# Optimization experiments

Measured on AMD Instinct MI355X. Metric: run time of the kernel, lower is better.

## Reference

```python
import jax, jax.numpy as jnp
import numpy as np

N_TOKENS = 8192
D_MODEL = 1024
D_HIDDEN = 4096
N_EXPERTS = 8
TOP_K = 2


def setup_inputs() -> dict:
    key = jax.random.key(0)
    ks = jax.random.split(key, 7)
    s = 0.02
    return {
        "x": jax.random.normal(ks[0], (N_TOKENS, D_MODEL), dtype=jnp.float32),
        "gate_w": jax.random.normal(ks[1], (D_MODEL, N_EXPERTS), dtype=jnp.float32) * s,
        "gate_b": jnp.zeros((N_EXPERTS,), dtype=jnp.float32),
        "w1": jax.random.normal(ks[2], (N_EXPERTS, D_MODEL, D_HIDDEN), dtype=jnp.float32) * s,
        "b1": jnp.zeros((N_EXPERTS, D_HIDDEN), dtype=jnp.float32),
        "w2": jax.random.normal(ks[3], (N_EXPERTS, D_HIDDEN, D_MODEL), dtype=jnp.float32) * s,
        "b2": jnp.zeros((N_EXPERTS, D_MODEL), dtype=jnp.float32),
    }


def reference(x, gate_w, gate_b, w1, b1, w2, b2):
    # Gating: softmax over experts, then top-k routing
    gate_scores = jax.nn.softmax(x @ gate_w + gate_b, axis=-1)        # [N, E]
    topk_vals, topk_idx = jax.lax.top_k(gate_scores, TOP_K)          # [N, K]

    # Combine weights: sum of topk_vals scattered to expert slots
    onehot = jax.nn.one_hot(topk_idx, N_EXPERTS, dtype=x.dtype)      # [N, K, E]
    combine = jnp.einsum('nk,nke->ne', topk_vals, onehot)            # [N, E]

    # Dense expert evaluation (math identical to masked dispatch: unselected
    # experts receive weight 0 in `combine`).
    h = jax.nn.relu(jnp.einsum('nd,edh->neh', x, w1) + b1)           # [N, E, H]
    expert_out = jnp.einsum('neh,ehd->ned', h, w2) + b2              # [N, E, D]
    output = jnp.einsum('ned,ne->nd', expert_out, combine)           # [N, D]

    # Load-balancing loss from routing counts
    load = jnp.sum(onehot, axis=(0, 1))                              # [E]
    load_balancing_loss = jnp.sum((load / jnp.sum(load)) ** 2)
    return output, load_balancing_loss
```

## Files before the change

### kernel.cpp

```cpp
#include <hip/hip_runtime.h>

#define D_MODEL   1024
#define D_HIDDEN  4096
#define N_EXPERTS 8
#define N_TOKENS  8192
#define NASSIGN   (N_TOKENS * 2)
#define PADCAP    (NASSIGN + N_EXPERTS * 128)
#define ROWT      (PADCAP / 128)

typedef unsigned short u16;
typedef __bf16 bf16x8 __attribute__((ext_vector_type(8)));
typedef float  f32x4  __attribute__((ext_vector_type(4)));

__device__ __forceinline__ u16 f2bf(float f) {
  union { float f; unsigned u; } c; c.f = f;
  unsigned u = c.u;
  u = (u + 0x7fffu + ((u >> 16) & 1u)) >> 16;
  return (u16)u;
}

__device__ __forceinline__ void async16(const void* g, void* l) {
  __builtin_amdgcn_global_load_lds(
      (const __attribute__((address_space(1))) unsigned int*)g,
      (__attribute__((address_space(3))) unsigned int*)l, 16, 0, 0);
}

__global__ __launch_bounds__(64) void gating_kernel(
    const float* __restrict__ x, const float* __restrict__ gw,
    const float* __restrict__ gb, int* __restrict__ counts,
    int* __restrict__ tok_idx, float* __restrict__ tok_w)
{
  const int n = blockIdx.x;
  const int lane = threadIdx.x;
  float acc[8] = {0.f,0.f,0.f,0.f,0.f,0.f,0.f,0.f};
  for (int d = lane; d < D_MODEL; d += 64) {
    float xv = x[(size_t)n * D_MODEL + d];
    const float4* g = (const float4*)&gw[d * 8];
    float4 g0 = g[0], g1 = g[1];
    acc[0] += xv * g0.x; acc[1] += xv * g0.y; acc[2] += xv * g0.z; acc[3] += xv * g0.w;
    acc[4] += xv * g1.x; acc[5] += xv * g1.y; acc[6] += xv * g1.z; acc[7] += xv * g1.w;
  }
  for (int off = 32; off; off >>= 1)
    #pragma unroll
    for (int e = 0; e < 8; ++e) acc[e] += __shfl_xor(acc[e], off, 64);
  if (lane == 0) {
    float l[8], p[8];
    float m = -1e30f;
    for (int e = 0; e < 8; ++e) { l[e] = acc[e] + gb[e]; m = fmaxf(m, l[e]); }
    float s = 0.f;
    for (int e = 0; e < 8; ++e) { p[e] = expf(l[e] - m); s += p[e]; }
    float inv = 1.f / s;
    for (int e = 0; e < 8; ++e) p[e] *= inv;
    int i0 = 0;
    for (int e = 1; e < 8; ++e) if (p[e] > p[i0]) i0 = e;
    int i1 = (i0 == 0) ? 1 : 0;
    for (int e = 0; e < 8; ++e) if (e != i0 && p[e] > p[i1]) i1 = e;
    tok_idx[2 * n]     = i0;  tok_idx[2 * n + 1] = i1;
    tok_w[2 * n]       = p[i0]; tok_w[2 * n + 1] = p[i1];
    atomicAdd(&counts[i0], 1);
    atomicAdd(&counts[i1], 1);
  }
}

__global__ void finalize_routing(const int* __restrict__ counts,
                                 int* __restrict__ offsets,
                                 float* __restrict__ out_loss)
{
  int off = 0;
  for (int e = 0; e < 8; ++e) {
    offsets[e] = off;
    off += ((counts[e] + 127) >> 7) << 7;
  }
  offsets[8] = off;
  float loss = 0.f;
  for (int e = 0; e < 8; ++e) {
    float f = (float)counts[e] * (1.f / (float)NASSIGN);
    loss += f * f;
  }
  *out_loss = loss;
}

__global__ __launch_bounds__(256) void scatter_kernel(
    const int* __restrict__ tok_idx, const float* __restrict__ tok_w,
    const int* __restrict__ offsets, int* __restrict__ cursors,
    int* __restrict__ assign_token, float* __restrict__ assign_w,
    int* __restrict__ tok_pos)
{
  const int n = blockIdx.x * 256 + threadIdx.x;
  #pragma unroll
  for (int k = 0; k < 2; ++k) {
    int e = tok_idx[n * 2 + k];
    int pos = offsets[e] + atomicAdd(&cursors[e], 1);
    assign_token[pos] = n;
    assign_w[pos] = tok_w[n * 2 + k];
    tok_pos[n * 2 + k] = pos;
  }
}

__global__ __launch_bounds__(256) void convert_x_kernel(
    const float* __restrict__ x, u16* __restrict__ xb)
{
  size_t i = ((size_t)blockIdx.x * 256 + threadIdx.x) * 4;
  float4 v = *(const float4*)&x[i];
  unsigned lo = (unsigned)f2bf(v.x) | ((unsigned)f2bf(v.y) << 16);
  unsigned hi = (unsigned)f2bf(v.z) | ((unsigned)f2bf(v.w) << 16);
  uint2 o; o.x = lo; o.y = hi;
  *(uint2*)&xb[i] = o;
}

__global__ __launch_bounds__(256) void transpose_cvt_kernel(
    const float* __restrict__ in, u16* __restrict__ out, int R, int C)
{
  const int e = blockIdx.z;
  const int c0 = blockIdx.x * 32, r0 = blockIdx.y * 32;
  __shared__ float tile[32][33];
  const int tx = threadIdx.x & 31, ty = threadIdx.x >> 5;
  const float* ip = in + (size_t)e * R * C;
  u16* op = out + (size_t)e * R * C;
  #pragma unroll
  for (int i = 0; i < 4; ++i)
    tile[ty + i * 8][tx] = ip[(size_t)(r0 + ty + i * 8) * C + c0 + tx];
  __syncthreads();
  #pragma unroll
  for (int i = 0; i < 4; ++i)
    op[(size_t)(c0 + ty + i * 8) * R + r0 + tx] = f2bf(tile[tx][ty + i * 8]);
}

__global__ __launch_bounds__(256) void gemm1_kernel(
    const u16* __restrict__ xb, const u16* __restrict__ w1t,
    const float* __restrict__ b1, const int* __restrict__ assign_token,
    const int* __restrict__ offsets, u16* __restrict__ hbuf)
{
  const int rt = blockIdx.x, ct = blockIdx.y;
  if (rt * 128 >= offsets[8]) return;
  int e = 0;
  while (offsets[e + 1] <= rt * 128) ++e;

  __shared__ __align__(16) u16 smem[16384];

  const int tid = threadIdx.x;
  const int wave = tid >> 6, lane = tid & 63;

  const int c0 = tid, c1 = tid + 256;
  const int r0 = c0 >> 2, s0 = c0 & 3;
  const int r1 = c1 >> 2, s1 = c1 & 3;
  const int sg0 = s0 ^ ((r0 >> 1) & 3);
  const int sg1 = s1 ^ ((r1 >> 1) & 3);

  const long aBase0 = (long)assign_token[rt * 128 + r0] * D_MODEL + sg0 * 8;
  const long aBase1 = (long)assign_token[rt * 128 + r1] * D_MODEL + sg1 * 8;
  const long bBase0 = ((long)e * D_HIDDEN + ct * 128 + r0) * D_MODEL + sg0 * 8;
  const long bBase1 = ((long)e * D_HIDDEN + ct * 128 + r1) * D_MODEL + sg1 * 8;

  const int wr = (wave >> 1) * 64, wc = (wave & 1) * 64;
  f32x4 acc[4][4];
  #pragma unroll
  for (int i = 0; i < 4; ++i)
    #pragma unroll
    for (int j = 0; j < 4; ++j) acc[i][j] = (f32x4){0.f, 0.f, 0.f, 0.f};

  int aoff[4], boff[4];
  #pragma unroll
  for (int i = 0; i < 4; ++i) {
    int row = wr + i * 16 + (lane & 15);
    aoff[i] = row * 32 + (((lane >> 4) ^ ((row >> 1) & 3)) * 8);
    int rown = wc + i * 16 + (lane & 15);
    boff[i] = rown * 32 + (((lane >> 4) ^ ((rown >> 1) & 3)) * 8);
  }

  #define STAGE1(p, k0) do { \
    u16* A_ = smem + (p) * 4096; \
    u16* B_ = smem + 8192 + (p) * 4096; \
    async16(xb  + aBase0 + (k0), A_ + wave * 512); \
    async16(xb  + aBase1 + (k0), A_ + 2048 + wave * 512); \
    async16(w1t + bBase0 + (k0), B_ + wave * 512); \
    async16(w1t + bBase1 + (k0), B_ + 2048 + wave * 512); \
  } while (0)

  STAGE1(0, 0);
  __syncthreads();
  int p = 0;
  for (int t = 0; t < D_MODEL / 32; ++t) {
    if (t < D_MODEL / 32 - 1) STAGE1(p ^ 1, (t + 1) * 32);
    const u16* A = smem + p * 4096;
    const u16* B = smem + 8192 + p * 4096;
    bf16x8 a[4], b[4];
    #pragma unroll
    for (int i = 0; i < 4; ++i) a[i] = *(const bf16x8*)&A[aoff[i]];
    #pragma unroll
    for (int j = 0; j < 4; ++j) b[j] = *(const bf16x8*)&B[boff[j]];
    #pragma unroll
    for (int i = 0; i < 4; ++i)
      #pragma unroll
      for (int j = 0; j < 4; ++j)
        acc[i][j] = __builtin_amdgcn_mfma_f32_16x16x32_bf16(a[i], b[j], acc[i][j], 0, 0, 0);
    __syncthreads();
    p ^= 1;
  }
  #undef STAGE1

  float bias[4];
  #pragma unroll
  for (int j = 0; j < 4; ++j)
    bias[j] = b1[(size_t)e * D_HIDDEN + ct * 128 + wc + j * 16 + (lane & 15)];

  u16* Hs = smem;
  #pragma unroll
  for (int i = 0; i < 4; ++i)
    #pragma unroll
    for (int j = 0; j < 4; ++j)
      #pragma unroll
      for (int r = 0; r < 4; ++r) {
        int rl = wr + i * 16 + ((lane >> 4) * 4) + r;
        int cl = wc + j * 16 + (lane & 15);
        Hs[rl * 128 + cl] = f2bf(fmaxf(acc[i][j][r] + bias[j], 0.f));
      }
  __syncthreads();
  #pragma unroll
  for (int t = 0; t < 8; ++t) {
    int cc = tid + t * 256;
    int row = cc >> 4, cs = cc & 15;
    *(uint4*)&hbuf[((size_t)(rt * 128 + row)) * D_HIDDEN + ct * 128 + cs * 8] =
        *(const uint4*)&Hs[row * 128 + cs * 8];
  }
}

template <bool EO>
__global__ __launch_bounds__(256) void gemm2_kernel(
    const u16* __restrict__ hbuf, const u16* __restrict__ w2t,
    const float* __restrict__ b2, const int* __restrict__ assign_token,
    const float* __restrict__ assign_w, const int* __restrict__ offsets,
    float* __restrict__ dst)
{
  const int rt = blockIdx.x, ct = blockIdx.y;
  if (rt * 128 >= offsets[8]) return;
  int e = 0;
  while (offsets[e + 1] <= rt * 128) ++e;

  __shared__ __align__(16) u16 smem[16384];
  __shared__ int tokS[128];
  __shared__ float wS[128];

  const int tid = threadIdx.x;
  const int wave = tid >> 6, lane = tid & 63;
  if (tid < 128) {
    tokS[tid] = assign_token[rt * 128 + tid];
    wS[tid] = assign_w[rt * 128 + tid];
  }

  const int c0 = tid, c1 = tid + 256;
  const int r0 = c0 >> 2, s0 = c0 & 3;
  const int r1 = c1 >> 2, s1 = c1 & 3;
  const int sg0 = s0 ^ ((r0 >> 1) & 3);
  const int sg1 = s1 ^ ((r1 >> 1) & 3);

  const long aBase0 = ((long)(rt * 128 + r0)) * D_HIDDEN + sg0 * 8;
  const long aBase1 = ((long)(rt * 128 + r1)) * D_HIDDEN + sg1 * 8;
  const long bBase0 = ((long)e * D_MODEL + ct * 128 + r0) * D_HIDDEN + sg0 * 8;
  const long bBase1 = ((long)e * D_MODEL + ct * 128 + r1) * D_HIDDEN + sg1 * 8;

  const int wr = (wave >> 1) * 64, wc = (wave & 1) * 64;
  f32x4 acc[4][4];
  #pragma unroll
  for (int i = 0; i < 4; ++i)
    #pragma unroll
    for (int j = 0; j < 4; ++j) acc[i][j] = (f32x4){0.f, 0.f, 0.f, 0.f};

  int aoff[4], boff[4];
  #pragma unroll
  for (int i = 0; i < 4; ++i) {
    int row = wr + i * 16 + (lane & 15);
    aoff[i] = row * 32 + (((lane >> 4) ^ ((row >> 1) & 3)) * 8);
    int rown = wc + i * 16 + (lane & 15);
    boff[i] = rown * 32 + (((lane >> 4) ^ ((rown >> 1) & 3)) * 8);
  }

  #define STAGE2(p, k0) do { \
    u16* A_ = smem + (p) * 4096; \
    u16* B_ = smem + 8192 + (p) * 4096; \
    async16(hbuf + aBase0 + (k0), A_ + wave * 512); \
    async16(hbuf + aBase1 + (k0), A_ + 2048 + wave * 512); \
    async16(w2t  + bBase0 + (k0), B_ + wave * 512); \
    async16(w2t  + bBase1 + (k0), B_ + 2048 + wave * 512); \
  } while (0)

  STAGE2(0, 0);
  __syncthreads();
  int p = 0;
  for (int t = 0; t < D_HIDDEN / 32; ++t) {
    if (t < D_HIDDEN / 32 - 1) STAGE2(p ^ 1, (t + 1) * 32);
    const u16* A = smem + p * 4096;
    const u16* B = smem + 8192 + p * 4096;
    bf16x8 a[4], b[4];
    #pragma unroll
    for (int i = 0; i < 4; ++i) a[i] = *(const bf16x8*)&A[aoff[i]];
    #pragma unroll
    for (int j = 0; j < 4; ++j) b[j] = *(const bf16x8*)&B[boff[j]];
    #pragma unroll
    for (int i = 0; i < 4; ++i)
      #pragma unroll
      for (int j = 0; j < 4; ++j)
        acc[i][j] = __builtin_amdgcn_mfma_f32_16x16x32_bf16(a[i], b[j], acc[i][j], 0, 0, 0);
    __syncthreads();
    p ^= 1;
  }
  #undef STAGE2

  float bias[4];
  #pragma unroll
  for (int j = 0; j < 4; ++j)
    bias[j] = b2[(size_t)e * D_MODEL + ct * 128 + wc + j * 16 + (lane & 15)];

  #pragma unroll
  for (int i = 0; i < 4; ++i)
    #pragma unroll
    for (int r = 0; r < 4; ++r) {
      int rl = wr + i * 16 + ((lane >> 4) * 4) + r;
      float wgt = wS[rl];
      if (EO) {
        size_t row = (size_t)(rt * 128 + rl);
        #pragma unroll
        for (int j = 0; j < 4; ++j) {
          float v = (acc[i][j][r] + bias[j]) * wgt;
          dst[row * D_MODEL + ct * 128 + wc + j * 16 + (lane & 15)] = v;
        }
      } else {
        int tok = tokS[rl];
        #pragma unroll
        for (int j = 0; j < 4; ++j) {
          float v = (acc[i][j][r] + bias[j]) * wgt;
          atomicAdd(&dst[(size_t)tok * D_MODEL + ct * 128 + wc + j * 16 + (lane & 15)], v);
        }
      }
    }
}

__global__ __launch_bounds__(256) void combine_kernel(
    const float* __restrict__ eo, const int* __restrict__ tok_pos,
    float* __restrict__ out)
{
  int idx = blockIdx.x * 256 + threadIdx.x;
  int n = idx >> 8;
  int c = (idx & 255) * 4;
  int p0 = tok_pos[2 * n], p1 = tok_pos[2 * n + 1];
  float4 a = *(const float4*)&eo[(size_t)p0 * D_MODEL + c];
  float4 b = *(const float4*)&eo[(size_t)p1 * D_MODEL + c];
  float4 o; o.x = a.x + b.x; o.y = a.y + b.y; o.z = a.z + b.z; o.w = a.w + b.w;
  *(float4*)&out[(size_t)n * D_MODEL + c] = o;
}

__global__ __launch_bounds__(256) void moe_fallback_kernel(
    const float* __restrict__ x, const float* __restrict__ w1,
    const float* __restrict__ b1, const float* __restrict__ w2,
    const float* __restrict__ b2, const int* __restrict__ tok_idx,
    const float* __restrict__ tok_w, float* __restrict__ out)
{
  const int a = blockIdx.x;
  const int n = a >> 1, slot = a & 1;
  const int e = tok_idx[n * 2 + slot];
  const float wgt = tok_w[n * 2 + slot];
  __shared__ float xs[D_MODEL];
  __shared__ float hs[D_HIDDEN];
  const int tid = threadIdx.x;
  for (int d = tid; d < D_MODEL; d += 256) xs[d] = x[(size_t)n * D_MODEL + d];
  __syncthreads();
  for (int h = tid; h < D_HIDDEN; h += 256) {
    float acc = b1[(size_t)e * D_HIDDEN + h];
    for (int d = 0; d < D_MODEL; ++d)
      acc += xs[d] * w1[((size_t)e * D_MODEL + d) * D_HIDDEN + h];
    hs[h] = fmaxf(acc, 0.f);
  }
  __syncthreads();
  for (int d = tid; d < D_MODEL; d += 256) {
    float acc = b2[(size_t)e * D_MODEL + d];
    for (int h = 0; h < D_HIDDEN; ++h)
      acc += hs[h] * w2[((size_t)e * D_HIDDEN + h) * D_MODEL + d];
    atomicAdd(&out[(size_t)n * D_MODEL + d], wgt * acc);
  }
}

extern "C" void kernel_launch(void* const* d_in, const int* in_sizes, int n_in,
                              void* d_out, int out_size, void* d_ws, size_t ws_size,
                              hipStream_t stream) {
  const float* x      = (const float*)d_in[0];
  const float* gate_w = (const float*)d_in[1];
  const float* gate_b = (const float*)d_in[2];
  const float* w1     = (const float*)d_in[3];
  const float* b1     = (const float*)d_in[4];
  const float* w2     = (const float*)d_in[5];
  const float* b2     = (const float*)d_in[6];
  float* out = (float*)d_out;

  char* ws = (char*)d_ws;
  int*   counts       = (int*)(ws + 0);
  int*   cursors      = (int*)(ws + 32);
  int*   offsets      = (int*)(ws + 64);
  int*   tok_idx      = (int*)(ws + 256);
  float* tok_w        = (float*)(ws + 65792);
  int*   tok_pos      = (int*)(ws + 131328);
  int*   assign_token = (int*)(ws + 196864);
  float* assign_w     = (float*)(ws + 266496);
  const size_t X0 = 336128;
  u16* xb   = (u16*)(ws + X0);
  u16* w1t  = (u16*)(ws + X0 + 16777216);
  u16* w2t  = (u16*)(ws + X0);
  u16* hbuf = (u16*)(ws + X0 + 83886080);
  float* eo = (float*)(ws + X0 + 226492416ull);
  const size_t REQ_FAST = X0 + 226492416ull;
  const size_t REQ_EO   = REQ_FAST + 71303168ull;

  const bool fast = (ws_size >= REQ_FAST);
  const bool eoPath = (ws_size >= REQ_EO);

  hipMemsetAsync(ws, 0, fast ? X0 : 336128, stream);
  if (!eoPath) {
    hipMemsetAsync(d_out, 0, (size_t)out_size * sizeof(float), stream);
  }

  gating_kernel<<<N_TOKENS, 64, 0, stream>>>(x, gate_w, gate_b, counts, tok_idx, tok_w);
  finalize_routing<<<1, 1, 0, stream>>>(counts, offsets, out + (out_size - 1));

  if (fast) {
    scatter_kernel<<<N_TOKENS / 256, 256, 0, stream>>>(tok_idx, tok_w, offsets, cursors,
                                                       assign_token, assign_w, tok_pos);
    convert_x_kernel<<<(N_TOKENS * D_MODEL) / 1024, 256, 0, stream>>>(x, xb);
    transpose_cvt_kernel<<<dim3(D_HIDDEN / 32, D_MODEL / 32, N_EXPERTS), 256, 0, stream>>>(
        w1, w1t, D_MODEL, D_HIDDEN);
    gemm1_kernel<<<dim3(ROWT, D_HIDDEN / 128), 256, 0, stream>>>(
        xb, w1t, b1, assign_token, offsets, hbuf);
    transpose_cvt_kernel<<<dim3(D_MODEL / 32, D_HIDDEN / 32, N_EXPERTS), 256, 0, stream>>>(
        w2, w2t, D_HIDDEN, D_MODEL);
    if (eoPath) {
      gemm2_kernel<true><<<dim3(ROWT, D_MODEL / 128), 256, 0, stream>>>(
          hbuf, w2t, b2, assign_token, assign_w, offsets, eo);
      combine_kernel<<<(N_TOKENS * D_MODEL) / 1024, 256, 0, stream>>>(eo, tok_pos, out);
    } else {
      gemm2_kernel<false><<<dim3(ROWT, D_MODEL / 128), 256, 0, stream>>>(
          hbuf, w2t, b2, assign_token, assign_w, offsets, out);
    }
  } else {
    moe_fallback_kernel<<<NASSIGN, 256, 0, stream>>>(x, w1, b1, w2, b2, tok_idx, tok_w, out);
  }
}
```

Baseline: 831.3 us.

## Triple-buffer LDS staging with vmcnt waits and one barrier per K-step in both GEMMs

Replaces the double-buffered async global-to-LDS pipeline in both expert GEMM kernels with a three-stage ring buffer. Loads are issued two steps ahead, and partial s_waitcnt vmcnt(4) lets the next stage's loads stay in flight while the current one is consumed. The loop drops one of its two __syncthreads, and the MFMA block runs at raised wave priority via s_setprio. LDS per block grows from 32KB to 48KB, which may lower occupancy, and correctness depends on the hand-tuned vmcnt count matching four loads per stage.

Result: slower. 858.8 us (+3.3%).

```diff
diff --git a/kernel.cpp b/kernel.cpp
--- a/kernel.cpp
+++ b/kernel.cpp
@@ -136,7 +136,7 @@
   int e = 0;
   while (offsets[e + 1] <= rt * 128) ++e;
 
-  __shared__ __align__(16) u16 smem[16384];
+  __shared__ __align__(16) u16 smem[24576];
 
   const int tid = threadIdx.x;
   const int wave = tid >> 6, lane = tid & 63;
@@ -168,34 +168,42 @@
     boff[i] = rown * 32 + (((lane >> 4) ^ ((rown >> 1) & 3)) * 8);
   }
 
-  #define STAGE1(p, k0) do { \
-    u16* A_ = smem + (p) * 4096; \
-    u16* B_ = smem + 8192 + (p) * 4096; \
+  #define STAGE1(bi, k0) do { \
+    u16* A_ = smem + (bi) * 4096; \
+    u16* B_ = smem + 12288 + (bi) * 4096; \
     async16(xb  + aBase0 + (k0), A_ + wave * 512); \
     async16(xb  + aBase1 + (k0), A_ + 2048 + wave * 512); \
     async16(w1t + bBase0 + (k0), B_ + wave * 512); \
     async16(w1t + bBase1 + (k0), B_ + 2048 + wave * 512); \
   } while (0)
 
+  const int NT = D_MODEL / 32;
   STAGE1(0, 0);
-  __syncthreads();
-  int p = 0;
-  for (int t = 0; t < D_MODEL / 32; ++t) {
-    if (t < D_MODEL / 32 - 1) STAGE1(p ^ 1, (t + 1) * 32);
-    const u16* A = smem + p * 4096;
-    const u16* B = smem + 8192 + p * 4096;
+  STAGE1(1, 32);
+  int bi = 0;
+  for (int t = 0; t < NT; ++t) {
+    if (t < NT - 1) asm volatile("s_waitcnt vmcnt(4)" ::: "memory");
+    else            asm volatile("s_waitcnt vmcnt(0)" ::: "memory");
+    __builtin_amdgcn_s_barrier();
+    const u16* A = smem + bi * 4096;
+    const u16* B = smem + 12288 + bi * 4096;
     bf16x8 a[4], b[4];
     #pragma unroll
     for (int i = 0; i < 4; ++i) a[i] = *(const bf16x8*)&A[aoff[i]];
     #pragma unroll
     for (int j = 0; j < 4; ++j) b[j] = *(const bf16x8*)&B[boff[j]];
+    __builtin_amdgcn_s_setprio(1);
     #pragma unroll
     for (int i = 0; i < 4; ++i)
       #pragma unroll
       for (int j = 0; j < 4; ++j)
         acc[i][j] = __builtin_amdgcn_mfma_f32_16x16x32_bf16(a[i], b[j], acc[i][j], 0, 0, 0);
-    __syncthreads();
-    p ^= 1;
+    __builtin_amdgcn_s_setprio(0);
+    if (t + 2 < NT) {
+      int nb = bi + 2; if (nb >= 3) nb -= 3;
+      STAGE1(nb, (t + 2) * 32);
+    }
+    ++bi; if (bi == 3) bi = 0;
   }
   #undef STAGE1
 
@@ -204,6 +212,7 @@
   for (int j = 0; j < 4; ++j)
     bias[j] = b1[(size_t)e * D_HIDDEN + ct * 128 + wc + j * 16 + (lane & 15)];
 
+  __syncthreads();
   u16* Hs = smem;
   #pragma unroll
   for (int i = 0; i < 4; ++i)
@@ -237,7 +246,7 @@
   int e = 0;
   while (offsets[e + 1] <= rt * 128) ++e;
 
-  __shared__ __align__(16) u16 smem[16384];
+  __shared__ __align__(16) u16 smem[24576];
   __shared__ int tokS[128];
   __shared__ float wS[128];
 
@@ -275,34 +284,42 @@
     boff[i] = rown * 32 + (((lane >> 4) ^ ((rown >> 1) & 3)) * 8);
   }
 
-  #define STAGE2(p, k0) do { \
-    u16* A_ = smem + (p) * 4096; \
-    u16* B_ = smem + 8192 + (p) * 4096; \
+  #define STAGE2(bi, k0) do { \
+    u16* A_ = smem + (bi) * 4096; \
+    u16* B_ = smem + 12288 + (bi) * 4096; \
     async16(hbuf + aBase0 + (k0), A_ + wave * 512); \
     async16(hbuf + aBase1 + (k0), A_ + 2048 + wave * 512); \
     async16(w2t  + bBase0 + (k0), B_ + wave * 512); \
     async16(w2t  + bBase1 + (k0), B_ + 2048 + wave * 512); \
   } while (0)
 
+  const int NT = D_HIDDEN / 32;
   STAGE2(0, 0);
-  __syncthreads();
-  int p = 0;
-  for (int t = 0; t < D_HIDDEN / 32; ++t) {
-    if (t < D_HIDDEN / 32 - 1) STAGE2(p ^ 1, (t + 1) * 32);
-    const u16* A = smem + p * 4096;
-    const u16* B = smem + 8192 + p * 4096;
+  STAGE2(1, 32);
+  int bi = 0;
+  for (int t = 0; t < NT; ++t) {
+    if (t < NT - 1) asm volatile("s_waitcnt vmcnt(4)" ::: "memory");
+    else            asm volatile("s_waitcnt vmcnt(0)" ::: "memory");
+    __builtin_amdgcn_s_barrier();
+    const u16* A = smem + bi * 4096;
+    const u16* B = smem + 12288 + bi * 4096;
     bf16x8 a[4], b[4];
     #pragma unroll
     for (int i = 0; i < 4; ++i) a[i] = *(const bf16x8*)&A[aoff[i]];
     #pragma unroll
     for (int j = 0; j < 4; ++j) b[j] = *(const bf16x8*)&B[boff[j]];
+    __builtin_amdgcn_s_setprio(1);
     #pragma unroll
     for (int i = 0; i < 4; ++i)
       #pragma unroll
       for (int j = 0; j < 4; ++j)
         acc[i][j] = __builtin_amdgcn_mfma_f32_16x16x32_bf16(a[i], b[j], acc[i][j], 0, 0, 0);
-    __syncthreads();
-    p ^= 1;
+    __builtin_amdgcn_s_setprio(0);
+    if (t + 2 < NT) {
+      int nb = bi + 2; if (nb >= 3) nb -= 3;
+      STAGE2(nb, (t + 2) * 32);
+    }
+    ++bi; if (bi == 3) bi = 0;
   }
   #undef STAGE2
 
```

## Enlarge GEMM tiles to 128x256 with BK=64 and 512-thread blocks

Applied to the files above, without the earlier changes.

Both expert GEMMs now use 8 waves per block, each block computing a 128x256 output tile, and step K by 64 with a wider XOR swizzle for LDS. MFMA sections are wrapped in s_setprio to favour issue. This raises data reuse per LDS byte and halves the number of K-loop barriers, at the cost of 96KB LDS per block and one block per CU. The gating kernel also packs four tokens per 256-thread block.

After: 828.0 us. Within noise of the previous version (-0.4%).

```diff
diff --git a/kernel.cpp b/kernel.cpp
--- a/kernel.cpp
+++ b/kernel.cpp
@@ -25,13 +25,13 @@
       (__attribute__((address_space(3))) unsigned int*)l, 16, 0, 0);
 }
 
-__global__ __launch_bounds__(64) void gating_kernel(
+__global__ __launch_bounds__(256) void gating_kernel(
     const float* __restrict__ x, const float* __restrict__ gw,
     const float* __restrict__ gb, int* __restrict__ counts,
     int* __restrict__ tok_idx, float* __restrict__ tok_w)
 {
-  const int n = blockIdx.x;
-  const int lane = threadIdx.x;
+  const int n = blockIdx.x * 4 + (threadIdx.x >> 6);
+  const int lane = threadIdx.x & 63;
   float acc[8] = {0.f,0.f,0.f,0.f,0.f,0.f,0.f,0.f};
   for (int d = lane; d < D_MODEL; d += 64) {
     float xv = x[(size_t)n * D_MODEL + d];
@@ -126,7 +126,8 @@
     op[(size_t)(c0 + ty + i * 8) * R + r0 + tx] = f2bf(tile[tx][ty + i * 8]);
 }
 
-__global__ __launch_bounds__(256) void gemm1_kernel(
+
+__global__ __launch_bounds__(512, 1) void gemm1_kernel(
     const u16* __restrict__ xb, const u16* __restrict__ w1t,
     const float* __restrict__ b1, const int* __restrict__ assign_token,
     const int* __restrict__ offsets, u16* __restrict__ hbuf)
@@ -136,73 +137,87 @@
   int e = 0;
   while (offsets[e + 1] <= rt * 128) ++e;
 
-  __shared__ __align__(16) u16 smem[16384];
-
+  __shared__ __align__(16) u16 smem[49152];
   const int tid = threadIdx.x;
   const int wave = tid >> 6, lane = tid & 63;
 
-  const int c0 = tid, c1 = tid + 256;
-  const int r0 = c0 >> 2, s0 = c0 & 3;
-  const int r1 = c1 >> 2, s1 = c1 & 3;
-  const int sg0 = s0 ^ ((r0 >> 1) & 3);
-  const int sg1 = s1 ^ ((r1 >> 1) & 3);
-
-  const long aBase0 = (long)assign_token[rt * 128 + r0] * D_MODEL + sg0 * 8;
-  const long aBase1 = (long)assign_token[rt * 128 + r1] * D_MODEL + sg1 * 8;
-  const long bBase0 = ((long)e * D_HIDDEN + ct * 128 + r0) * D_MODEL + sg0 * 8;
-  const long bBase1 = ((long)e * D_HIDDEN + ct * 128 + r1) * D_MODEL + sg1 * 8;
-
-  const int wr = (wave >> 1) * 64, wc = (wave & 1) * 64;
+  const int arow0 = tid >> 3;
+  const int aslot0 = (tid & 7) ^ (arow0 & 7);
+  const int ac1 = tid + 512;
+  const int arow1 = ac1 >> 3;
+  const int aslot1 = (ac1 & 7) ^ (arow1 & 7);
+  const long aBase0 = (long)assign_token[rt * 128 + arow0] * D_MODEL + aslot0 * 8;
+  const long aBase1 = (long)assign_token[rt * 128 + arow1] * D_MODEL + aslot1 * 8;
+
+  long bBase[4];
+  #pragma unroll
+  for (int k = 0; k < 4; ++k) {
+    int c = tid + k * 512;
+    int r = c >> 3, s = (c & 7) ^ (r & 7);
+    bBase[k] = ((long)e * D_HIDDEN + ct * 256 + r) * D_MODEL + s * 8;
+  }
+
+  const int wr = (wave >> 2) * 64;
+  const int wc = (wave & 3) * 64;
   f32x4 acc[4][4];
   #pragma unroll
   for (int i = 0; i < 4; ++i)
     #pragma unroll
     for (int j = 0; j < 4; ++j) acc[i][j] = (f32x4){0.f, 0.f, 0.f, 0.f};
 
-  int aoff[4], boff[4];
+  int aro[4], asz[4], bro[4], bsz[4];
   #pragma unroll
   for (int i = 0; i < 4; ++i) {
     int row = wr + i * 16 + (lane & 15);
-    aoff[i] = row * 32 + (((lane >> 4) ^ ((row >> 1) & 3)) * 8);
-    int rown = wc + i * 16 + (lane & 15);
-    boff[i] = rown * 32 + (((lane >> 4) ^ ((rown >> 1) & 3)) * 8);
-  }
-
-  #define STAGE1(p, k0) do { \
-    u16* A_ = smem + (p) * 4096; \
-    u16* B_ = smem + 8192 + (p) * 4096; \
-    async16(xb  + aBase0 + (k0), A_ + wave * 512); \
-    async16(xb  + aBase1 + (k0), A_ + 2048 + wave * 512); \
-    async16(w1t + bBase0 + (k0), B_ + wave * 512); \
-    async16(w1t + bBase1 + (k0), B_ + 2048 + wave * 512); \
+    aro[i] = row * 64; asz[i] = row & 7;
+    int col = wc + i * 16 + (lane & 15);
+    bro[i] = col * 64; bsz[i] = col & 7;
+  }
+  const int lh = lane >> 4;
+
+  #define STG1(p, k0) do { \
+    u16* A_ = smem + (p) * 8192; \
+    u16* B_ = smem + 16384 + (p) * 16384; \
+    async16(xb  + aBase0   + (k0), A_ + wave * 512); \
+    async16(xb  + aBase1   + (k0), A_ + 4096 + wave * 512); \
+    async16(w1t + bBase[0] + (k0), B_ + wave * 512); \
+    async16(w1t + bBase[1] + (k0), B_ + 4096 + wave * 512); \
+    async16(w1t + bBase[2] + (k0), B_ + 8192 + wave * 512); \
+    async16(w1t + bBase[3] + (k0), B_ + 12288 + wave * 512); \
   } while (0)
 
-  STAGE1(0, 0);
-  __syncthreads();
-  int p = 0;
-  for (int t = 0; t < D_MODEL / 32; ++t) {
-    if (t < D_MODEL / 32 - 1) STAGE1(p ^ 1, (t + 1) * 32);
-    const u16* A = smem + p * 4096;
-    const u16* B = smem + 8192 + p * 4096;
-    bf16x8 a[4], b[4];
-    #pragma unroll
-    for (int i = 0; i < 4; ++i) a[i] = *(const bf16x8*)&A[aoff[i]];
-    #pragma unroll
-    for (int j = 0; j < 4; ++j) b[j] = *(const bf16x8*)&B[boff[j]];
+  const int NT = D_MODEL / 64;
+  STG1(0, 0);
+  __syncthreads();
+  for (int t = 0; t < NT; ++t) {
+    if (t + 1 < NT) STG1((t + 1) & 1, (t + 1) * 64);
+    const u16* A = smem + (t & 1) * 8192;
+    const u16* B = smem + 16384 + (t & 1) * 16384;
+    bf16x8 a[2][4], b[2][4];
+    #pragma unroll
+    for (int i = 0; i < 4; ++i) {
+      a[0][i] = *(const bf16x8*)&A[aro[i] + ((lh       ^ asz[i]) * 8)];
+      a[1][i] = *(const bf16x8*)&A[aro[i] + (((4 | lh) ^ asz[i]) * 8)];
+      b[0][i] = *(const bf16x8*)&B[bro[i] + ((lh       ^ bsz[i]) * 8)];
+      b[1][i] = *(const bf16x8*)&B[bro[i] + (((4 | lh) ^ bsz[i]) * 8)];
+    }
+    __builtin_amdgcn_s_setprio(1);
     #pragma unroll
     for (int i = 0; i < 4; ++i)
       #pragma unroll
-      for (int j = 0; j < 4; ++j)
-        acc[i][j] = __builtin_amdgcn_mfma_f32_16x16x32_bf16(a[i], b[j], acc[i][j], 0, 0, 0);
+      for (int j = 0; j < 4; ++j) {
+        acc[i][j] = __builtin_amdgcn_mfma_f32_16x16x32_bf16(a[0][i], b[0][j], acc[i][j], 0, 0, 0);
+        acc[i][j] = __builtin_amdgcn_mfma_f32_16x16x32_bf16(a[1][i], b[1][j], acc[i][j], 0, 0, 0);
+      }
+    __builtin_amdgcn_s_setprio(0);
     __syncthreads();
-    p ^= 1;
-  }
-  #undef STAGE1
+  }
+  #undef STG1
 
   float bias[4];
   #pragma unroll
   for (int j = 0; j < 4; ++j)
-    bias[j] = b1[(size_t)e * D_HIDDEN + ct * 128 + wc + j * 16 + (lane & 15)];
+    bias[j] = b1[(size_t)e * D_HIDDEN + ct * 256 + wc + j * 16 + (lane & 15)];
 
   u16* Hs = smem;
   #pragma unroll
@@ -213,20 +228,20 @@
       for (int r = 0; r < 4; ++r) {
         int rl = wr + i * 16 + ((lane >> 4) * 4) + r;
         int cl = wc + j * 16 + (lane & 15);
-        Hs[rl * 128 + cl] = f2bf(fmaxf(acc[i][j][r] + bias[j], 0.f));
+        Hs[rl * 256 + cl] = f2bf(fmaxf(acc[i][j][r] + bias[j], 0.f));
       }
   __syncthreads();
   #pragma unroll
   for (int t = 0; t < 8; ++t) {
-    int cc = tid + t * 256;
-    int row = cc >> 4, cs = cc & 15;
-    *(uint4*)&hbuf[((size_t)(rt * 128 + row)) * D_HIDDEN + ct * 128 + cs * 8] =
-        *(const uint4*)&Hs[row * 128 + cs * 8];
+    int cc = tid + t * 512;
+    int row = cc >> 5, cs = cc & 31;
+    *(uint4*)&hbuf[((size_t)(rt * 128 + row)) * D_HIDDEN + ct * 256 + cs * 8] =
+        *(const uint4*)&Hs[row * 256 + cs * 8];
   }
 }
 
 template <bool EO>
-__global__ __launch_bounds__(256) void gemm2_kernel(
+__global__ __launch_bounds__(512, 1) void gemm2_kernel(
     const u16* __restrict__ hbuf, const u16* __restrict__ w2t,
     const float* __restrict__ b2, const int* __restrict__ assign_token,
     const float* __restrict__ assign_w, const int* __restrict__ offsets,
@@ -237,7 +252,7 @@
   int e = 0;
   while (offsets[e + 1] <= rt * 128) ++e;
 
-  __shared__ __align__(16) u16 smem[16384];
+  __shared__ __align__(16) u16 smem[49152];
   __shared__ int tokS[128];
   __shared__ float wS[128];
 
@@ -248,68 +263,83 @@
     wS[tid] = assign_w[rt * 128 + tid];
   }
 
-  const int c0 = tid, c1 = tid + 256;
-  const int r0 = c0 >> 2, s0 = c0 & 3;
-  const int r1 = c1 >> 2, s1 = c1 & 3;
-  const int sg0 = s0 ^ ((r0 >> 1) & 3);
-  const int sg1 = s1 ^ ((r1 >> 1) & 3);
-
-  const long aBase0 = ((long)(rt * 128 + r0)) * D_HIDDEN + sg0 * 8;
-  const long aBase1 = ((long)(rt * 128 + r1)) * D_HIDDEN + sg1 * 8;
-  const long bBase0 = ((long)e * D_MODEL + ct * 128 + r0) * D_HIDDEN + sg0 * 8;
-  const long bBase1 = ((long)e * D_MODEL + ct * 128 + r1) * D_HIDDEN + sg1 * 8;
-
-  const int wr = (wave >> 1) * 64, wc = (wave & 1) * 64;
+  const int arow0 = tid >> 3;
+  const int aslot0 = (tid & 7) ^ (arow0 & 7);
+  const int ac1 = tid + 512;
+  const int arow1 = ac1 >> 3;
+  const int aslot1 = (ac1 & 7) ^ (arow1 & 7);
+  const long aBase0 = ((long)(rt * 128 + arow0)) * D_HIDDEN + aslot0 * 8;
+  const long aBase1 = ((long)(rt * 128 + arow1)) * D_HIDDEN + aslot1 * 8;
+
+  long bBase[4];
+  #pragma unroll
+  for (int k = 0; k < 4; ++k) {
+    int c = tid + k * 512;
+    int r = c >> 3, s = (c & 7) ^ (r & 7);
+    bBase[k] = ((long)e * D_MODEL + ct * 256 + r) * D_HIDDEN + s * 8;
+  }
+
+  const int wr = (wave >> 2) * 64;
+  const int wc = (wave & 3) * 64;
   f32x4 acc[4][4];
   #pragma unroll
   for (int i = 0; i < 4; ++i)
     #pragma unroll
     for (int j = 0; j < 4; ++j) acc[i][j] = (f32x4){0.f, 0.f, 0.f, 0.f};
 
-  int aoff[4], boff[4];
+  int aro[4], asz[4], bro[4], bsz[4];
   #pragma unroll
   for (int i = 0; i < 4; ++i) {
     int row = wr + i * 16 + (lane & 15);
-    aoff[i] = row * 32 + (((lane >> 4) ^ ((row >> 1) & 3)) * 8);
-    int rown = wc + i * 16 + (lane & 15);
-    boff[i] = rown * 32 + (((lane >> 4) ^ ((rown >> 1) & 3)) * 8);
-  }
-
-  #define STAGE2(p, k0) do { \
-    u16* A_ = smem + (p) * 4096; \
-    u16* B_ = smem + 8192 + (p) * 4096; \
-    async16(hbuf + aBase0 + (k0), A_ + wave * 512); \
-    async16(hbuf + aBase1 + (k0), A_ + 2048 + wave * 512); \
-    async16(w2t  + bBase0 + (k0), B_ + wave * 512); \
-    async16(w2t  + bBase1 + (k0), B_ + 2048 + wave * 512); \
+    aro[i] = row * 64; asz[i] = row & 7;
+    int col = wc + i * 16 + (lane & 15);
+    bro[i] = col * 64; bsz[i] = col & 7;
+  }
+  const int lh = lane >> 4;
+
+  #define STG2(p, k0) do { \
+    u16* A_ = smem + (p) * 8192; \
+    u16* B_ = smem + 16384 + (p) * 16384; \
+    async16(hbuf + aBase0   + (k0), A_ + wave * 512); \
+    async16(hbuf + aBase1   + (k0), A_ + 4096 + wave * 512); \
+    async16(w2t  + bBase[0] + (k0), B_ + wave * 512); \
+    async16(w2t  + bBase[1] + (k0), B_ + 4096 + wave * 512); \
+    async16(w2t  + bBase[2] + (k0), B_ + 8192 + wave * 512); \
+    async16(w2t  + bBase[3] + (k0), B_ + 12288 + wave * 512); \
   } while (0)
 
-  STAGE2(0, 0);
-  __syncthreads();
-  int p = 0;
-  for (int t = 0; t < D_HIDDEN / 32; ++t) {
-    if (t < D_HIDDEN / 32 - 1) STAGE2(p ^ 1, (t + 1) * 32);
-    const u16* A = smem + p * 4096;
-    const u16* B = smem + 8192 + p * 4096;
-    bf16x8 a[4], b[4];
-    #pragma unroll
-    for (int i = 0; i < 4; ++i) a[i] = *(const bf16x8*)&A[aoff[i]];
-    #pragma unroll
-    for (int j = 0; j < 4; ++j) b[j] = *(const bf16x8*)&B[boff[j]];
+  const int NT = D_HIDDEN / 64;
+  STG2(0, 0);
+  __syncthreads();
+  for (int t = 0; t < NT; ++t) {
+    if (t + 1 < NT) STG2((t + 1) & 1, (t + 1) * 64);
+    const u16* A = smem + (t & 1) * 8192;
+    const u16* B = smem + 16384 + (t & 1) * 16384;
+    bf16x8 a[2][4], b[2][4];
+    #pragma unroll
+    for (int i = 0; i < 4; ++i) {
+      a[0][i] = *(const bf16x8*)&A[aro[i] + ((lh       ^ asz[i]) * 8)];
+      a[1][i] = *(const bf16x8*)&A[aro[i] + (((4 | lh) ^ asz[i]) * 8)];
+      b[0][i] = *(const bf16x8*)&B[bro[i] + ((lh       ^ bsz[i]) * 8)];
+      b[1][i] = *(const bf16x8*)&B[bro[i] + (((4 | lh) ^ bsz[i]) * 8)];
+    }
+    __builtin_amdgcn_s_setprio(1);
     #pragma unroll
     for (int i = 0; i < 4; ++i)
       #pragma unroll
-      for (int j = 0; j < 4; ++j)
-        acc[i][j] = __builtin_amdgcn_mfma_f32_16x16x32_bf16(a[i], b[j], acc[i][j], 0, 0, 0);
+      for (int j = 0; j < 4; ++j) {
+        acc[i][j] = __builtin_amdgcn_mfma_f32_16x16x32_bf16(a[0][i], b[0][j], acc[i][j], 0, 0, 0);
+        acc[i][j] = __builtin_amdgcn_mfma_f32_16x16x32_bf16(a[1][i], b[1][j], acc[i][j], 0, 0, 0);
+      }
+    __builtin_amdgcn_s_setprio(0);
     __syncthreads();
-    p ^= 1;
-  }
-  #undef STAGE2
+  }
+  #undef STG2
 
   float bias[4];
   #pragma unroll
   for (int j = 0; j < 4; ++j)
-    bias[j] = b2[(size_t)e * D_MODEL + ct * 128 + wc + j * 16 + (lane & 15)];
+    bias[j] = b2[(size_t)e * D_MODEL + ct * 256 + wc + j * 16 + (lane & 15)];
 
   #pragma unroll
   for (int i = 0; i < 4; ++i)
@@ -322,14 +352,14 @@
         #pragma unroll
         for (int j = 0; j < 4; ++j) {
           float v = (acc[i][j][r] + bias[j]) * wgt;
-          dst[row * D_MODEL + ct * 128 + wc + j * 16 + (lane & 15)] = v;
+          dst[row * D_MODEL + ct * 256 + wc + j * 16 + (lane & 15)] = v;
         }
       } else {
         int tok = tokS[rl];
         #pragma unroll
         for (int j = 0; j < 4; ++j) {
           float v = (acc[i][j][r] + bias[j]) * wgt;
-          atomicAdd(&dst[(size_t)tok * D_MODEL + ct * 128 + wc + j * 16 + (lane & 15)], v);
+          atomicAdd(&dst[(size_t)tok * D_MODEL + ct * 256 + wc + j * 16 + (lane & 15)], v);
         }
       }
     }
@@ -417,7 +447,7 @@
     hipMemsetAsync(d_out, 0, (size_t)out_size * sizeof(float), stream);
   }
 
-  gating_kernel<<<N_TOKENS, 64, 0, stream>>>(x, gate_w, gate_b, counts, tok_idx, tok_w);
+  gating_kernel<<<N_TOKENS / 4, 256, 0, stream>>>(x, gate_w, gate_b, counts, tok_idx, tok_w);
   finalize_routing<<<1, 1, 0, stream>>>(counts, offsets, out + (out_size - 1));
 
   if (fast) {
@@ -426,16 +456,16 @@
     convert_x_kernel<<<(N_TOKENS * D_MODEL) / 1024, 256, 0, stream>>>(x, xb);
     transpose_cvt_kernel<<<dim3(D_HIDDEN / 32, D_MODEL / 32, N_EXPERTS), 256, 0, stream>>>(
         w1, w1t, D_MODEL, D_HIDDEN);
-    gemm1_kernel<<<dim3(ROWT, D_HIDDEN / 128), 256, 0, stream>>>(
+    gemm1_kernel<<<dim3(ROWT, D_HIDDEN / 256), 512, 0, stream>>>(
         xb, w1t, b1, assign_token, offsets, hbuf);
     transpose_cvt_kernel<<<dim3(D_MODEL / 32, D_HIDDEN / 32, N_EXPERTS), 256, 0, stream>>>(
         w2, w2t, D_HIDDEN, D_MODEL);
     if (eoPath) {
-      gemm2_kernel<true><<<dim3(ROWT, D_MODEL / 128), 256, 0, stream>>>(
+      gemm2_kernel<true><<<dim3(ROWT, D_MODEL / 256), 512, 0, stream>>>(
           hbuf, w2t, b2, assign_token, assign_w, offsets, eo);
       combine_kernel<<<(N_TOKENS * D_MODEL) / 1024, 256, 0, stream>>>(eo, tok_pos, out);
     } else {
-      gemm2_kernel<false><<<dim3(ROWT, D_MODEL / 128), 256, 0, stream>>>(
+      gemm2_kernel<false><<<dim3(ROWT, D_MODEL / 256), 512, 0, stream>>>(
           hbuf, w2t, b2, assign_token, assign_w, offsets, out);
     }
   } else {
```
